# Optimization experiments

Hardware: AMD Instinct MI355X
Metric: run time of the kernel (lower is better)

Reference implementation:

```python
import jax, jax.numpy as jnp
import numpy as np

B, C, H, W = 4, 64, 64, 64
DQ = 64            # query/key dim (hardcoded 64 in the module)
FP_DIM = 128       # fingerprint_dim
SCALE = 1.0 / 8.0  # 1/sqrt(64)


def setup_inputs() -> dict:
    key = jax.random.key(0)
    ks = jax.random.split(key, 12)
    s = 0.05
    return {
        "x": jax.random.normal(ks[0], (B, C, H, W), jnp.float32),
        "fingerprint": jax.random.normal(ks[1], (B, FP_DIM), jnp.float32),
        # 1x1 conv weights stored as [out_ch, in_ch]
        "Wq": jax.random.normal(ks[2], (DQ, C), jnp.float32) * s,
        "bq": jax.random.normal(ks[3], (DQ,), jnp.float32) * s,
        "Wk": jax.random.normal(ks[4], (DQ, C), jnp.float32) * s,
        "bk": jax.random.normal(ks[5], (DQ,), jnp.float32) * s,
        "Wv": jax.random.normal(ks[6], (C, C), jnp.float32) * s,
        "bv": jax.random.normal(ks[7], (C,), jnp.float32) * s,
        "Wo": jax.random.normal(ks[8], (C, C), jnp.float32) * s,
        "bo": jax.random.normal(ks[9], (C,), jnp.float32) * s,
        "Wfp": jax.random.normal(ks[10], (DQ, FP_DIM), jnp.float32) * s,
        "bfp": jax.random.normal(ks[11], (DQ,), jnp.float32) * s,
    }


def reference(x, fingerprint, Wq, bq, Wk, bk, Wv, bv, Wo, bo, Wfp, bfp):
    b, c, h, w = x.shape
    # fingerprint projection: Linear(fingerprint_dim, 64)
    fp_proj = fingerprint @ Wfp.T + bfp                      # [B, 64]
    # 1x1 convs as channel einsums
    q = jnp.einsum('bchw,oc->bohw', x, Wq) + bq[None, :, None, None]  # [B,64,H,W]
    k = jnp.einsum('bchw,oc->bohw', x, Wk) + bk[None, :, None, None]  # [B,64,H,W]
    v = jnp.einsum('bchw,oc->bohw', x, Wv) + bv[None, :, None, None]  # [B,C,H,W]
    qf = q.reshape(b, DQ, h * w)   # [B,64,N]
    kf = k.reshape(b, DQ, h * w)   # [B,64,N]
    vf = v.reshape(b, c, h * w)    # [B,C,N]
    # attn[b,i,j] = <q_i, k_j>/sqrt(64), softmax over keys j
    attn = jax.nn.softmax(jnp.einsum('bdi,bdj->bij', qf, kf) * SCALE, axis=2)  # [B,N,N]
    out = jnp.einsum('bcj,bij->bci', vf, attn).reshape(b, c, h, w)
    # fingerprint-gated modulation map
    attn_map = jax.nn.sigmoid(jnp.einsum('bdhw,bd->bhw', q, fp_proj))[:, None]  # [B,1,H,W]
    out = out * attn_map + x
    out = jnp.einsum('bchw,oc->bohw', out, Wo) + bo[None, :, None, None]
    return out
```

## Files before the change

kernel.cpp:

```cpp
#include <hip/hip_runtime.h>
#include <cstdint>
#include <cstddef>

#define B_    4
#define C_    64
#define N_    4096
#define FPD_  128
#define QSCALE_ (0.125f * 1.4426950408889634f)

typedef short bf16x8 __attribute__((ext_vector_type(8)));
typedef float f32x4  __attribute__((ext_vector_type(4)));

__device__ inline unsigned short f2bf(float f) {
    union { float f; unsigned int u; } v; v.f = f;
    unsigned int u = v.u;
    return (unsigned short)((u + 0x7FFFu + ((u >> 16) & 1u)) >> 16);
}
__device__ inline unsigned int pack2bf(float a, float b) {
    return (unsigned int)f2bf(a) | ((unsigned int)f2bf(b) << 16);
}
__device__ inline unsigned short f2bf_fast(float f) {
    union { float f; unsigned int u; } v; v.f = f;
    return (unsigned short)((v.u + 0x8000u) >> 16);
}

__global__ __launch_bounds__(256) void qkv_kernel(
    const float* __restrict__ x,
    const float* __restrict__ Wq, const float* __restrict__ bq,
    const float* __restrict__ Wk, const float* __restrict__ bk,
    const float* __restrict__ Wv, const float* __restrict__ bv,
    const float* __restrict__ fp, const float* __restrict__ Wfp,
    const float* __restrict__ bfp,
    float* __restrict__ gate,
    unsigned short* __restrict__ Qb, unsigned short* __restrict__ Kb,
    unsigned short* __restrict__ Vb)
{
    __shared__ unsigned short xT[64 * 72];
    __shared__ unsigned short Wl[64 * 72];
    __shared__ unsigned short rp[64 * 72];
    __shared__ float gredf[256];
    __shared__ float fpp[64];

    int tid  = threadIdx.x;
    int bx   = blockIdx.x;
    int pass = bx >> 8;
    int rem  = bx & 255;
    int b  = rem >> 6;
    int p0 = (rem & 63) << 6;
    const float* xb = x + (size_t)b * (C_ * N_) + p0;

    const float* Wsrc = (pass == 0) ? Wq : (pass == 1) ? Wk : Wv;
    const float* bsrc = (pass == 0) ? bq : (pass == 1) ? bk : bv;
    float wscale = (pass == 0) ? QSCALE_ : 1.0f;

    {
        int o  = tid >> 2;
        int cb = (tid & 3) << 4;
        const float4* src = reinterpret_cast<const float4*>(&Wsrc[o * 64 + cb]);
        float4 w0 = src[0], w1 = src[1], w2 = src[2], w3 = src[3];
        uint4 lo, hi;
        lo.x = pack2bf(w0.x * wscale, w0.y * wscale);
        lo.y = pack2bf(w0.z * wscale, w0.w * wscale);
        lo.z = pack2bf(w1.x * wscale, w1.y * wscale);
        lo.w = pack2bf(w1.z * wscale, w1.w * wscale);
        hi.x = pack2bf(w2.x * wscale, w2.y * wscale);
        hi.y = pack2bf(w2.z * wscale, w2.w * wscale);
        hi.z = pack2bf(w3.x * wscale, w3.y * wscale);
        hi.w = pack2bf(w3.z * wscale, w3.w * wscale);
        *reinterpret_cast<uint4*>(&Wl[o * 72 + cb])     = lo;
        *reinterpret_cast<uint4*>(&Wl[o * 72 + cb + 8]) = hi;
    }
    for (int i = 0; i < 16; ++i) {
        int l = tid + i * 256;
        int c = l >> 6, p = l & 63;
        xT[p * 72 + c] = f2bf(xb[(size_t)c * N_ + p]);
    }
    if (pass == 0) {
        int d = tid >> 2, kq = tid & 3;
        const float4* wrow = reinterpret_cast<const float4*>(&Wfp[d * FPD_ + kq * 32]);
        const float4* frow = reinterpret_cast<const float4*>(&fp[b * FPD_ + kq * 32]);
        float s = 0.f;
        #pragma unroll
        for (int i = 0; i < 8; ++i) {
            float4 w4 = wrow[i], f4 = frow[i];
            s += w4.x * f4.x + w4.y * f4.y + w4.z * f4.z + w4.w * f4.w;
        }
        gredf[tid] = s;
    }
    __syncthreads();
    if (pass == 0 && tid < 64)
        fpp[tid] = bfp[tid] + gredf[tid * 4] + gredf[tid * 4 + 1]
                 + gredf[tid * 4 + 2] + gredf[tid * 4 + 3];
    if (pass == 0) __syncthreads();

    int lane = tid & 63;
    int wv   = __builtin_amdgcn_readfirstlane(tid >> 6);
    int quad = lane >> 4, l16 = lane & 15;
    int prow = wv * 16 + l16;

    bf16x8 bx0 = *reinterpret_cast<bf16x8*>(&xT[prow * 72 + quad * 8]);
    bf16x8 bx1 = *reinterpret_cast<bf16x8*>(&xT[prow * 72 + 32 + quad * 8]);

    float gp = 0.f;
    #pragma unroll
    for (int t4 = 0; t4 < 4; ++t4) {
        bf16x8 a0 = *reinterpret_cast<bf16x8*>(&Wl[(t4 * 16 + l16) * 72 + quad * 8]);
        bf16x8 a1 = *reinterpret_cast<bf16x8*>(&Wl[(t4 * 16 + l16) * 72 + 32 + quad * 8]);
        f32x4 c4 = (f32x4){0.f, 0.f, 0.f, 0.f};
        c4 = __builtin_amdgcn_mfma_f32_16x16x32_bf16(a0, bx0, c4, 0, 0, 0);
        c4 = __builtin_amdgcn_mfma_f32_16x16x32_bf16(a1, bx1, c4, 0, 0, 0);
        float4 bias = *reinterpret_cast<const float4*>(&bsrc[t4 * 16 + quad * 4]);
        c4[0] += bias.x * wscale; c4[1] += bias.y * wscale;
        c4[2] += bias.z * wscale; c4[3] += bias.w * wscale;
        if (pass == 0) {
            gp = fmaf(c4[0], fpp[t4 * 16 + quad * 4 + 0], gp);
            gp = fmaf(c4[1], fpp[t4 * 16 + quad * 4 + 1], gp);
            gp = fmaf(c4[2], fpp[t4 * 16 + quad * 4 + 2], gp);
            gp = fmaf(c4[3], fpp[t4 * 16 + quad * 4 + 3], gp);
        }
        if (pass < 2) {
            int dd = t4 * 16 + quad * 4;
            *reinterpret_cast<ushort2*>(&rp[prow * 72 + dd]) =
                (ushort2){f2bf(c4[0]), f2bf(c4[1])};
            *reinterpret_cast<ushort2*>(&rp[prow * 72 + dd + 2]) =
                (ushort2){f2bf(c4[2]), f2bf(c4[3])};
        } else {
            #pragma unroll
            for (int j = 0; j < 4; ++j)
                rp[(t4 * 16 + quad * 4 + j) * 72 + prow] = f2bf(c4[j]);
        }
    }
    if (pass == 0) {
        gp += __shfl_xor(gp, 16);
        gp += __shfl_xor(gp, 32);
        if (lane < 16) {
            int pos = p0 + wv * 16 + lane;
            float s = gp * (1.0f / QSCALE_);
            gate[b * N_ + pos] = 1.f / (1.f + __expf(-s));
        }
    }
    __syncthreads();

    int row = tid >> 2;
    int cb  = (tid & 3) << 4;
    ushort4 u[4];
    #pragma unroll
    for (int k = 0; k < 4; ++k)
        u[k] = *reinterpret_cast<ushort4*>(&rp[row * 72 + cb + k * 4]);
    unsigned short* dst;
    if (pass == 0)      dst = Qb + ((size_t)b * N_ + p0 + row) * 64 + cb;
    else if (pass == 1) dst = Kb + ((size_t)b * N_ + p0 + row) * 64 + cb;
    else                dst = Vb + ((size_t)b * 64 + row) * N_ + p0 + cb;
    #pragma unroll
    for (int k = 0; k < 4; ++k)
        *reinterpret_cast<ushort4*>(dst + k * 4) = u[k];
}

__global__ __launch_bounds__(256, 4) void attn_kernel(
    const unsigned short* __restrict__ Qb, const unsigned short* __restrict__ Kb,
    const unsigned short* __restrict__ Vb, float* __restrict__ Opart,
    float* __restrict__ lpart)
{
    __shared__ unsigned short Ks[64 * 72];
    __shared__ unsigned short Vs[64 * 72];
    __shared__ unsigned short Ps[64 * 72];

    int tid = threadIdx.x;
    int bx  = blockIdx.x;
    int qt  = bx >> 4;
    int grp = bx & 15;
    int b   = grp >> 2;
    int ks  = grp & 3;
    int q0  = qt << 6;
    int kbase = ks << 10;

    int lane = tid & 63;
    int wv   = __builtin_amdgcn_readfirstlane(tid >> 6);
    int quad = lane >> 4, l16 = lane & 15;
    int qs0  = wv << 4;

    const unsigned short* Qg = Qb + ((size_t)b * N_ + q0) * 64;
    bf16x8 aq0 = *reinterpret_cast<const bf16x8*>(&Qg[(qs0 + l16) * 64 + quad * 8]);
    bf16x8 aq1 = *reinterpret_cast<const bf16x8*>(&Qg[(qs0 + l16) * 64 + 32 + quad * 8]);

    const unsigned short* Kg = Kb + ((size_t)b * N_ + kbase) * 64;
    const unsigned short* Vg = Vb + (size_t)b * 64 * N_ + kbase;

    int r0 = tid >> 4;
    int cc = (tid & 15) << 2;

    ushort4 kr[4], vr[4];
    #pragma unroll
    for (int i = 0; i < 4; ++i) {
        int r = r0 + 16 * i;
        kr[i] = *reinterpret_cast<const ushort4*>(&Kg[(size_t)r * 64 + cc]);
        vr[i] = *reinterpret_cast<const ushort4*>(&Vg[(size_t)r * N_ + cc]);
    }

    f32x4 oacc[4]; f32x4 lacc = (f32x4){0.f, 0.f, 0.f, 0.f};
    #pragma unroll
    for (int cs = 0; cs < 4; ++cs) oacc[cs] = (f32x4){0.f, 0.f, 0.f, 0.f};
    bf16x8 ones;
    #pragma unroll
    for (int i = 0; i < 8; ++i) ones[i] = (short)0x3F80;

    for (int kt = 0; kt < 16; ++kt) {
        __syncthreads();
        #pragma unroll
        for (int i = 0; i < 4; ++i) {
            int r = r0 + 16 * i;
            *reinterpret_cast<ushort4*>(&Ks[r * 72 + cc]) = kr[i];
            *reinterpret_cast<ushort4*>(&Vs[r * 72 + cc]) = vr[i];
        }
        __syncthreads();
        if (kt < 15) {
            int kk = (kt + 1) << 6;
            #pragma unroll
            for (int i = 0; i < 4; ++i) {
                int r = r0 + 16 * i;
                kr[i] = *reinterpret_cast<const ushort4*>(&Kg[(size_t)(kk + r) * 64 + cc]);
                vr[i] = *reinterpret_cast<const ushort4*>(&Vg[(size_t)r * N_ + kk + cc]);
            }
        }

        #pragma unroll
        for (int kj = 0; kj < 4; ++kj) {
            bf16x8 bk0 = *reinterpret_cast<bf16x8*>(&Ks[(kj * 16 + l16) * 72 + quad * 8]);
            bf16x8 bk1 = *reinterpret_cast<bf16x8*>(&Ks[(kj * 16 + l16) * 72 + 32 + quad * 8]);
            f32x4 s = (f32x4){0.f, 0.f, 0.f, 0.f};
            s = __builtin_amdgcn_mfma_f32_16x16x32_bf16(aq0, bk0, s, 0, 0, 0);
            s = __builtin_amdgcn_mfma_f32_16x16x32_bf16(aq1, bk1, s, 0, 0, 0);
            #pragma unroll
            for (int j = 0; j < 4; ++j) {
                float pv = exp2f(s[j]);
                Ps[(qs0 + quad * 4 + j) * 72 + kj * 16 + l16] = f2bf_fast(pv);
            }
        }
        __asm__ volatile("s_waitcnt lgkmcnt(0)" ::: "memory");

        bf16x8 ap0 = *reinterpret_cast<bf16x8*>(&Ps[(qs0 + l16) * 72 + quad * 8]);
        bf16x8 ap1 = *reinterpret_cast<bf16x8*>(&Ps[(qs0 + l16) * 72 + 32 + quad * 8]);
        lacc = __builtin_amdgcn_mfma_f32_16x16x32_bf16(ap0, ones, lacc, 0, 0, 0);
        lacc = __builtin_amdgcn_mfma_f32_16x16x32_bf16(ap1, ones, lacc, 0, 0, 0);
        #pragma unroll
        for (int cs = 0; cs < 4; ++cs) {
            bf16x8 bv0 = *reinterpret_cast<bf16x8*>(&Vs[(cs * 16 + l16) * 72 + quad * 8]);
            bf16x8 bv1 = *reinterpret_cast<bf16x8*>(&Vs[(cs * 16 + l16) * 72 + 32 + quad * 8]);
            oacc[cs] = __builtin_amdgcn_mfma_f32_16x16x32_bf16(ap0, bv0, oacc[cs], 0, 0, 0);
            oacc[cs] = __builtin_amdgcn_mfma_f32_16x16x32_bf16(ap1, bv1, oacc[cs], 0, 0, 0);
        }
    }

    float* Og = Opart + (((size_t)ks * B_ + b) * N_ + q0) * 64;
    #pragma unroll
    for (int j = 0; j < 4; ++j) {
        int row = qs0 + quad * 4 + j;
        #pragma unroll
        for (int cs = 0; cs < 4; ++cs)
            Og[row * 64 + cs * 16 + l16] = oacc[cs][j];
    }
    if (l16 == 0) {
        #pragma unroll
        for (int j = 0; j < 4; ++j)
            lpart[((size_t)ks * B_ + b) * N_ + q0 + qs0 + quad * 4 + j] = lacc[j];
    }
}

__global__ __launch_bounds__(256) void epi_kernel(
    const float* __restrict__ Opart, const float* __restrict__ lpart,
    const float* __restrict__ x, const float* __restrict__ gate,
    const float* __restrict__ Wo, const float* __restrict__ bo,
    float* __restrict__ out)
{
    __shared__ float xs[64 * 68];
    __shared__ float osum[64 * 68];
    __shared__ unsigned short Wl[32 * 72];
    __shared__ float os[32 * 68];

    int tid  = threadIdx.x;
    int bx   = blockIdx.x;
    int half = bx >> 8;
    int rem  = bx & 255;
    int b  = rem >> 6;
    int p0 = (rem & 63) << 6;
    const float* xb = x + (size_t)b * (C_ * N_) + p0;

    for (int i = 0; i < 16; ++i) {
        int l = tid + i * 256;
        int c = l >> 6, p = l & 63;
        xs[p * 68 + c] = xb[(size_t)c * N_ + p];
    }
    {
        const float* Ob = Opart + ((size_t)b * N_ + p0) * 64;
        const size_t kstride = (size_t)B_ * N_ * 64;
        #pragma unroll
        for (int i = 0; i < 4; ++i) {
            int u = tid + i * 256;
            int p = u >> 4, c4 = (u & 15) << 2;
            size_t off = (size_t)p * 64 + c4;
            float4 a0 = *reinterpret_cast<const float4*>(&Ob[off]);
            float4 a1 = *reinterpret_cast<const float4*>(&Ob[off + kstride]);
            float4 a2 = *reinterpret_cast<const float4*>(&Ob[off + 2 * kstride]);
            float4 a3 = *reinterpret_cast<const float4*>(&Ob[off + 3 * kstride]);
            float4 ssum;
            ssum.x = (a0.x + a1.x) + (a2.x + a3.x);
            ssum.y = (a0.y + a1.y) + (a2.y + a3.y);
            ssum.z = (a0.z + a1.z) + (a2.z + a3.z);
            ssum.w = (a0.w + a1.w) + (a2.w + a3.w);
            *reinterpret_cast<float4*>(&osum[p * 68 + c4]) = ssum;
        }
    }
    {
        int ol = tid >> 3;
        int cb = (tid & 7) << 3;
        const float4* src = reinterpret_cast<const float4*>(
            &Wo[(half * 32 + ol) * 64 + cb]);
        float4 w0 = src[0], w1 = src[1];
        uint2 pkd;
        pkd.x = pack2bf(w0.x, w0.y); pkd.y = pack2bf(w0.z, w0.w);
        *reinterpret_cast<uint2*>(&Wl[ol * 72 + cb]) = pkd;
        pkd.x = pack2bf(w1.x, w1.y); pkd.y = pack2bf(w1.z, w1.w);
        *reinterpret_cast<uint2*>(&Wl[ol * 72 + cb + 4]) = pkd;
    }
    __syncthreads();

    int lane = tid & 63;
    int wv   = __builtin_amdgcn_readfirstlane(tid >> 6);
    int quad = lane >> 4, l16 = lane & 15;
    int prow = wv * 16 + l16;
    int pos  = p0 + prow;

    float lv = lpart[(size_t)b * N_ + pos]
             + lpart[((size_t)B_ + b) * N_ + pos]
             + lpart[(2 * (size_t)B_ + b) * N_ + pos]
             + lpart[(3 * (size_t)B_ + b) * N_ + pos];
    float gi = gate[b * N_ + pos] / lv;

    bf16x8 bt[2];
    #pragma unroll
    for (int chunk = 0; chunk < 2; ++chunk) {
        int cb2 = chunk * 32 + quad * 8;
        float4 oa = *reinterpret_cast<float4*>(&osum[prow * 68 + cb2]);
        float4 ob4 = *reinterpret_cast<float4*>(&osum[prow * 68 + cb2 + 4]);
        float4 xa = *reinterpret_cast<float4*>(&xs[prow * 68 + cb2]);
        float4 xb4 = *reinterpret_cast<float4*>(&xs[prow * 68 + cb2 + 4]);
        bt[chunk][0] = f2bf(fmaf(oa.x, gi, xa.x));
        bt[chunk][1] = f2bf(fmaf(oa.y, gi, xa.y));
        bt[chunk][2] = f2bf(fmaf(oa.z, gi, xa.z));
        bt[chunk][3] = f2bf(fmaf(oa.w, gi, xa.w));
        bt[chunk][4] = f2bf(fmaf(ob4.x, gi, xb4.x));
        bt[chunk][5] = f2bf(fmaf(ob4.y, gi, xb4.y));
        bt[chunk][6] = f2bf(fmaf(ob4.z, gi, xb4.z));
        bt[chunk][7] = f2bf(fmaf(ob4.w, gi, xb4.w));
    }

    #pragma unroll
    for (int tt = 0; tt < 2; ++tt) {
        int ot = half * 2 + tt;
        bf16x8 a0 = *reinterpret_cast<bf16x8*>(&Wl[(tt * 16 + l16) * 72 + quad * 8]);
        bf16x8 a1 = *reinterpret_cast<bf16x8*>(&Wl[(tt * 16 + l16) * 72 + 32 + quad * 8]);
        f32x4 c4 = (f32x4){0.f, 0.f, 0.f, 0.f};
        c4 = __builtin_amdgcn_mfma_f32_16x16x32_bf16(a0, bt[0], c4, 0, 0, 0);
        c4 = __builtin_amdgcn_mfma_f32_16x16x32_bf16(a1, bt[1], c4, 0, 0, 0);
        float4 bias = *reinterpret_cast<const float4*>(&bo[ot * 16 + quad * 4]);
        c4[0] += bias.x; c4[1] += bias.y; c4[2] += bias.z; c4[3] += bias.w;
        #pragma unroll
        for (int j = 0; j < 4; ++j)
            os[(tt * 16 + quad * 4 + j) * 68 + prow] = c4[j];
    }
    __syncthreads();

    int row = tid >> 3;
    int pb  = (tid & 7) << 3;
    float* ob = out + ((size_t)b * 64 + half * 32 + row) * N_ + p0 + pb;
    *reinterpret_cast<float4*>(ob)     = *reinterpret_cast<float4*>(&os[row * 68 + pb]);
    *reinterpret_cast<float4*>(ob + 4) = *reinterpret_cast<float4*>(&os[row * 68 + pb + 4]);
}

extern "C" void kernel_launch(void* const* d_in, const int* in_sizes, int n_in,
                              void* d_out, int out_size, void* d_ws, size_t ws_size,
                              hipStream_t stream)
{
    const float* x   = (const float*)d_in[0];
    const float* fp  = (const float*)d_in[1];
    const float* Wq  = (const float*)d_in[2];
    const float* bq  = (const float*)d_in[3];
    const float* Wk  = (const float*)d_in[4];
    const float* bk  = (const float*)d_in[5];
    const float* Wv  = (const float*)d_in[6];
    const float* bv  = (const float*)d_in[7];
    const float* Wo  = (const float*)d_in[8];
    const float* bo  = (const float*)d_in[9];
    const float* Wfp = (const float*)d_in[10];
    const float* bfp = (const float*)d_in[11];
    float* out = (float*)d_out;

    char* ws = (char*)d_ws;
    float* gate = (float*)(ws);
    unsigned short* Qb = (unsigned short*)(ws + 65536);
    unsigned short* Kb = (unsigned short*)(ws + 65536 + 2097152);
    unsigned short* Vb = (unsigned short*)(ws + 65536 + 2 * 2097152);
    float* Opart = (float*)(ws + 65536 + 3 * 2097152);
    float* lpart = (float*)(ws + 65536 + 3 * 2097152 + 16777216);


    hipLaunchKernelGGL(qkv_kernel, dim3(768), dim3(256), 0, stream,
                       x, Wq, bq, Wk, bk, Wv, bv, fp, Wfp, bfp,
                       gate, Qb, Kb, Vb);
    hipLaunchKernelGGL(attn_kernel, dim3(1024), dim3(256), 0, stream,
                       Qb, Kb, Vb, Opart, lpart);
    hipLaunchKernelGGL(epi_kernel, dim3(512), dim3(256), 0, stream,
                       Opart, lpart, x, gate, Wo, bo, out);
}
```

Before: 129.0 us.

## Double query tile per attention block, store partial outputs in bf16, vectorize x loads

The attention kernel now handles 128 queries per block (32 per wave), so each K/V tile staged in shared memory is reused across twice as many queries, and the grid is halved. Partial outputs are written as bf16 instead of fp32, halving the traffic of the split-K partial buffer that the epilogue reads back. The x transpose loads in the qkv and epilogue kernels now use float4 reads, and exp2 uses the hardware builtin. Risks include higher register pressure, since launch bounds drop to 2 blocks per CU, fewer blocks to fill the GPU, and extra rounding error from bf16 partials.

```diff
diff --git a/kernel.cpp b/kernel.cpp
--- a/kernel.cpp
+++ b/kernel.cpp
@@ -8,6 +8,12 @@
 #define FPD_  128
 #define QSCALE_ (0.125f * 1.4426950408889634f)
 
+#if __has_builtin(__builtin_amdgcn_exp2f)
+#define EXP2(x) __builtin_amdgcn_exp2f(x)
+#else
+#define EXP2(x) exp2f(x)
+#endif
+
 typedef short bf16x8 __attribute__((ext_vector_type(8)));
 typedef float f32x4  __attribute__((ext_vector_type(4)));
 
@@ -22,6 +28,12 @@
 __device__ inline unsigned short f2bf_fast(float f) {
     union { float f; unsigned int u; } v; v.f = f;
     return (unsigned short)((v.u + 0x8000u) >> 16);
+}
+__device__ inline float bflo(unsigned int u) {
+    union { unsigned int u; float f; } v; v.u = u << 16; return v.f;
+}
+__device__ inline float bfhi(unsigned int u) {
+    union { unsigned int u; float f; } v; v.u = u & 0xFFFF0000u; return v.f;
 }
 
 __global__ __launch_bounds__(256) void qkv_kernel(
@@ -70,10 +82,15 @@
         *reinterpret_cast<uint4*>(&Wl[o * 72 + cb])     = lo;
         *reinterpret_cast<uint4*>(&Wl[o * 72 + cb + 8]) = hi;
     }
-    for (int i = 0; i < 16; ++i) {
-        int l = tid + i * 256;
-        int c = l >> 6, p = l & 63;
-        xT[p * 72 + c] = f2bf(xb[(size_t)c * N_ + p]);
+    #pragma unroll
+    for (int i = 0; i < 4; ++i) {
+        int u = tid + i * 256;
+        int c = u >> 4, p4 = (u & 15) << 2;
+        float4 v = *reinterpret_cast<const float4*>(&xb[(size_t)c * N_ + p4]);
+        xT[(p4 + 0) * 72 + c] = f2bf(v.x);
+        xT[(p4 + 1) * 72 + c] = f2bf(v.y);
+        xT[(p4 + 2) * 72 + c] = f2bf(v.z);
+        xT[(p4 + 3) * 72 + c] = f2bf(v.w);
     }
     if (pass == 0) {
         int d = tid >> 2, kq = tid & 3;
@@ -156,14 +173,14 @@
         *reinterpret_cast<ushort4*>(dst + k * 4) = u[k];
 }
 
-__global__ __launch_bounds__(256, 4) void attn_kernel(
+__global__ __launch_bounds__(256, 2) void attn_kernel(
     const unsigned short* __restrict__ Qb, const unsigned short* __restrict__ Kb,
-    const unsigned short* __restrict__ Vb, float* __restrict__ Opart,
+    const unsigned short* __restrict__ Vb, unsigned short* __restrict__ Opart,
     float* __restrict__ lpart)
 {
     __shared__ unsigned short Ks[64 * 72];
     __shared__ unsigned short Vs[64 * 72];
-    __shared__ unsigned short Ps[64 * 72];
+    __shared__ unsigned short Ps[128 * 72];
 
     int tid = threadIdx.x;
     int bx  = blockIdx.x;
@@ -171,17 +188,23 @@
     int grp = bx & 15;
     int b   = grp >> 2;
     int ks  = grp & 3;
-    int q0  = qt << 6;
+    int q0  = qt << 7;
     int kbase = ks << 10;
 
     int lane = tid & 63;
     int wv   = __builtin_amdgcn_readfirstlane(tid >> 6);
     int quad = lane >> 4, l16 = lane & 15;
-    int qs0  = wv << 4;
+    int qs0  = wv << 5;
 
     const unsigned short* Qg = Qb + ((size_t)b * N_ + q0) * 64;
-    bf16x8 aq0 = *reinterpret_cast<const bf16x8*>(&Qg[(qs0 + l16) * 64 + quad * 8]);
-    bf16x8 aq1 = *reinterpret_cast<const bf16x8*>(&Qg[(qs0 + l16) * 64 + 32 + quad * 8]);
+    bf16x8 aq[2][2];
+    #pragma unroll
+    for (int s = 0; s < 2; ++s) {
+        aq[s][0] = *reinterpret_cast<const bf16x8*>(
+            &Qg[(qs0 + s * 16 + l16) * 64 + quad * 8]);
+        aq[s][1] = *reinterpret_cast<const bf16x8*>(
+            &Qg[(qs0 + s * 16 + l16) * 64 + 32 + quad * 8]);
+    }
 
     const unsigned short* Kg = Kb + ((size_t)b * N_ + kbase) * 64;
     const unsigned short* Vg = Vb + (size_t)b * 64 * N_ + kbase;
@@ -197,9 +220,13 @@
         vr[i] = *reinterpret_cast<const ushort4*>(&Vg[(size_t)r * N_ + cc]);
     }
 
-    f32x4 oacc[4]; f32x4 lacc = (f32x4){0.f, 0.f, 0.f, 0.f};
-    #pragma unroll
-    for (int cs = 0; cs < 4; ++cs) oacc[cs] = (f32x4){0.f, 0.f, 0.f, 0.f};
+    f32x4 oacc[2][4]; f32x4 lacc[2];
+    #pragma unroll
+    for (int s = 0; s < 2; ++s) {
+        lacc[s] = (f32x4){0.f, 0.f, 0.f, 0.f};
+        #pragma unroll
+        for (int cs = 0; cs < 4; ++cs) oacc[s][cs] = (f32x4){0.f, 0.f, 0.f, 0.f};
+    }
     bf16x8 ones;
     #pragma unroll
     for (int i = 0; i < 8; ++i) ones[i] = (short)0x3F80;
@@ -227,47 +254,62 @@
         for (int kj = 0; kj < 4; ++kj) {
             bf16x8 bk0 = *reinterpret_cast<bf16x8*>(&Ks[(kj * 16 + l16) * 72 + quad * 8]);
             bf16x8 bk1 = *reinterpret_cast<bf16x8*>(&Ks[(kj * 16 + l16) * 72 + 32 + quad * 8]);
-            f32x4 s = (f32x4){0.f, 0.f, 0.f, 0.f};
-            s = __builtin_amdgcn_mfma_f32_16x16x32_bf16(aq0, bk0, s, 0, 0, 0);
-            s = __builtin_amdgcn_mfma_f32_16x16x32_bf16(aq1, bk1, s, 0, 0, 0);
-            #pragma unroll
-            for (int j = 0; j < 4; ++j) {
-                float pv = exp2f(s[j]);
-                Ps[(qs0 + quad * 4 + j) * 72 + kj * 16 + l16] = f2bf_fast(pv);
+            #pragma unroll
+            for (int s = 0; s < 2; ++s) {
+                f32x4 sv = (f32x4){0.f, 0.f, 0.f, 0.f};
+                sv = __builtin_amdgcn_mfma_f32_16x16x32_bf16(aq[s][0], bk0, sv, 0, 0, 0);
+                sv = __builtin_amdgcn_mfma_f32_16x16x32_bf16(aq[s][1], bk1, sv, 0, 0, 0);
+                #pragma unroll
+                for (int j = 0; j < 4; ++j) {
+                    float pv = EXP2(sv[j]);
+                    Ps[(qs0 + s * 16 + quad * 4 + j) * 72 + kj * 16 + l16] = f2bf_fast(pv);
+                }
             }
         }
         __asm__ volatile("s_waitcnt lgkmcnt(0)" ::: "memory");
 
-        bf16x8 ap0 = *reinterpret_cast<bf16x8*>(&Ps[(qs0 + l16) * 72 + quad * 8]);
-        bf16x8 ap1 = *reinterpret_cast<bf16x8*>(&Ps[(qs0 + l16) * 72 + 32 + quad * 8]);
-        lacc = __builtin_amdgcn_mfma_f32_16x16x32_bf16(ap0, ones, lacc, 0, 0, 0);
-        lacc = __builtin_amdgcn_mfma_f32_16x16x32_bf16(ap1, ones, lacc, 0, 0, 0);
+        bf16x8 ap[2][2];
+        #pragma unroll
+        for (int s = 0; s < 2; ++s) {
+            ap[s][0] = *reinterpret_cast<bf16x8*>(&Ps[(qs0 + s * 16 + l16) * 72 + quad * 8]);
+            ap[s][1] = *reinterpret_cast<bf16x8*>(&Ps[(qs0 + s * 16 + l16) * 72 + 32 + quad * 8]);
+            lacc[s] = __builtin_amdgcn_mfma_f32_16x16x32_bf16(ap[s][0], ones, lacc[s], 0, 0, 0);
+            lacc[s] = __builtin_amdgcn_mfma_f32_16x16x32_bf16(ap[s][1], ones, lacc[s], 0, 0, 0);
+        }
         #pragma unroll
         for (int cs = 0; cs < 4; ++cs) {
             bf16x8 bv0 = *reinterpret_cast<bf16x8*>(&Vs[(cs * 16 + l16) * 72 + quad * 8]);
             bf16x8 bv1 = *reinterpret_cast<bf16x8*>(&Vs[(cs * 16 + l16) * 72 + 32 + quad * 8]);
-            oacc[cs] = __builtin_amdgcn_mfma_f32_16x16x32_bf16(ap0, bv0, oacc[cs], 0, 0, 0);
-            oacc[cs] = __builtin_amdgcn_mfma_f32_16x16x32_bf16(ap1, bv1, oacc[cs], 0, 0, 0);
-        }
-    }
-
-    float* Og = Opart + (((size_t)ks * B_ + b) * N_ + q0) * 64;
-    #pragma unroll
-    for (int j = 0; j < 4; ++j) {
-        int row = qs0 + quad * 4 + j;
-        #pragma unroll
-        for (int cs = 0; cs < 4; ++cs)
-            Og[row * 64 + cs * 16 + l16] = oacc[cs][j];
-    }
+            #pragma unroll
+            for (int s = 0; s < 2; ++s) {
+                oacc[s][cs] = __builtin_amdgcn_mfma_f32_16x16x32_bf16(ap[s][0], bv0, oacc[s][cs], 0, 0, 0);
+                oacc[s][cs] = __builtin_amdgcn_mfma_f32_16x16x32_bf16(ap[s][1], bv1, oacc[s][cs], 0, 0, 0);
+            }
+        }
+    }
+
+    unsigned short* Og = Opart + (((size_t)ks * B_ + b) * N_ + q0) * 64;
+    #pragma unroll
+    for (int s = 0; s < 2; ++s)
+        #pragma unroll
+        for (int j = 0; j < 4; ++j) {
+            int row = qs0 + s * 16 + quad * 4 + j;
+            #pragma unroll
+            for (int cs = 0; cs < 4; ++cs)
+                Og[row * 64 + cs * 16 + l16] = f2bf_fast(oacc[s][cs][j]);
+        }
     if (l16 == 0) {
         #pragma unroll
-        for (int j = 0; j < 4; ++j)
-            lpart[((size_t)ks * B_ + b) * N_ + q0 + qs0 + quad * 4 + j] = lacc[j];
+        for (int s = 0; s < 2; ++s)
+            #pragma unroll
+            for (int j = 0; j < 4; ++j)
+                lpart[((size_t)ks * B_ + b) * N_ + q0 + qs0 + s * 16 + quad * 4 + j]
+                    = lacc[s][j];
     }
 }
 
 __global__ __launch_bounds__(256) void epi_kernel(
-    const float* __restrict__ Opart, const float* __restrict__ lpart,
+    const unsigned short* __restrict__ Opart, const float* __restrict__ lpart,
     const float* __restrict__ x, const float* __restrict__ gate,
     const float* __restrict__ Wo, const float* __restrict__ bo,
     float* __restrict__ out)
@@ -285,28 +327,33 @@
     int p0 = (rem & 63) << 6;
     const float* xb = x + (size_t)b * (C_ * N_) + p0;
 
-    for (int i = 0; i < 16; ++i) {
-        int l = tid + i * 256;
-        int c = l >> 6, p = l & 63;
-        xs[p * 68 + c] = xb[(size_t)c * N_ + p];
+    #pragma unroll
+    for (int i = 0; i < 4; ++i) {
+        int u = tid + i * 256;
+        int c = u >> 4, p4 = (u & 15) << 2;
+        float4 v = *reinterpret_cast<const float4*>(&xb[(size_t)c * N_ + p4]);
+        xs[(p4 + 0) * 68 + c] = v.x;
+        xs[(p4 + 1) * 68 + c] = v.y;
+        xs[(p4 + 2) * 68 + c] = v.z;
+        xs[(p4 + 3) * 68 + c] = v.w;
     }
     {
-        const float* Ob = Opart + ((size_t)b * N_ + p0) * 64;
+        const unsigned short* Ob = Opart + ((size_t)b * N_ + p0) * 64;
         const size_t kstride = (size_t)B_ * N_ * 64;
         #pragma unroll
         for (int i = 0; i < 4; ++i) {
             int u = tid + i * 256;
             int p = u >> 4, c4 = (u & 15) << 2;
             size_t off = (size_t)p * 64 + c4;
-            float4 a0 = *reinterpret_cast<const float4*>(&Ob[off]);
-            float4 a1 = *reinterpret_cast<const float4*>(&Ob[off + kstride]);
-            float4 a2 = *reinterpret_cast<const float4*>(&Ob[off + 2 * kstride]);
-            float4 a3 = *reinterpret_cast<const float4*>(&Ob[off + 3 * kstride]);
+            uint2 a0 = *reinterpret_cast<const uint2*>(&Ob[off]);
+            uint2 a1 = *reinterpret_cast<const uint2*>(&Ob[off + kstride]);
+            uint2 a2 = *reinterpret_cast<const uint2*>(&Ob[off + 2 * kstride]);
+            uint2 a3 = *reinterpret_cast<const uint2*>(&Ob[off + 3 * kstride]);
             float4 ssum;
-            ssum.x = (a0.x + a1.x) + (a2.x + a3.x);
-            ssum.y = (a0.y + a1.y) + (a2.y + a3.y);
-            ssum.z = (a0.z + a1.z) + (a2.z + a3.z);
-            ssum.w = (a0.w + a1.w) + (a2.w + a3.w);
+            ssum.x = (bflo(a0.x) + bflo(a1.x)) + (bflo(a2.x) + bflo(a3.x));
+            ssum.y = (bfhi(a0.x) + bfhi(a1.x)) + (bfhi(a2.x) + bfhi(a3.x));
+            ssum.z = (bflo(a0.y) + bflo(a1.y)) + (bflo(a2.y) + bflo(a3.y));
+            ssum.w = (bfhi(a0.y) + bfhi(a1.y)) + (bfhi(a2.y) + bfhi(a3.y));
             *reinterpret_cast<float4*>(&osum[p * 68 + c4]) = ssum;
         }
     }
@@ -400,14 +447,14 @@
     unsigned short* Qb = (unsigned short*)(ws + 65536);
     unsigned short* Kb = (unsigned short*)(ws + 65536 + 2097152);
     unsigned short* Vb = (unsigned short*)(ws + 65536 + 2 * 2097152);
-    float* Opart = (float*)(ws + 65536 + 3 * 2097152);
-    float* lpart = (float*)(ws + 65536 + 3 * 2097152 + 16777216);
+    unsigned short* Opart = (unsigned short*)(ws + 65536 + 3 * 2097152);
+    float* lpart = (float*)(ws + 65536 + 3 * 2097152 + 8388608);
 
 
     hipLaunchKernelGGL(qkv_kernel, dim3(768), dim3(256), 0, stream,
                        x, Wq, bq, Wk, bk, Wv, bv, fp, Wfp, bfp,
                        gate, Qb, Kb, Vb);
-    hipLaunchKernelGGL(attn_kernel, dim3(1024), dim3(256), 0, stream,
+    hipLaunchKernelGGL(attn_kernel, dim3(512), dim3(256), 0, stream,
                        Qb, Kb, Vb, Opart, lpart);
     hipLaunchKernelGGL(epi_kernel, dim3(512), dim3(256), 0, stream,
                        Opart, lpart, x, gate, Wo, bo, out);
```

Measured after the change: 118.6 us. 8.0% less time.
